# Optimization experiments

Hardware: AMD Instinct MI355X
Metric: run time of the kernel (lower is better)

The kernel has to match this reference:

```python
import jax, jax.numpy as jnp
import numpy as np
import math

D_MODEL = 512
KEY_DIM = 128
NUM_LAYERS = 2
TEMP = 30.0
NORM_EPS = 1e-5
NORM_SCALE = math.sqrt(1.0 / (D_MODEL * 4 * 4))


def _l2norm_lastdim(x):
    # F.normalize(x, p=2, dim=-1): x / max(||x||, 1e-12)
    n = jnp.sqrt(jnp.sum(x * x, axis=-1, keepdims=True))
    return x / jnp.maximum(n, 1e-12)


def _attn(q, k, v, WK, bK):
    # q: [Sq,B,D], k: [Sk,B,D], v: [Sk,B,D] -> [Sq,B,D]
    wq = _l2norm_lastdim(q @ WK + bK)            # [Sq,B,K]
    wk = _l2norm_lastdim(k @ WK + bK)            # [Sk,B,K]
    dot = jnp.einsum('qbk,sbk->bqs', wq, wk)     # cosine sims
    aff = jax.nn.softmax(dot * TEMP, axis=-1)
    return jnp.einsum('bqs,sbd->qbd', aff, v)


def _instance_norm(x, h, w):
    # x: [HW,B,D]; InstanceL2Norm over (D,h,w) per batch element, size_average=True
    HW, B, D = x.shape
    ss = jnp.sum(x * x, axis=(0, 2))             # [B]
    factor = NORM_SCALE * jnp.sqrt((D * h * w) / (ss + NORM_EPS))
    return x * factor[None, :, None]


def _encoder(src4d, WKs, bKs):
    B, D, H, W = src4d.shape
    x = src4d.reshape(B, D, H * W).transpose(2, 0, 1)   # [HW,B,D]
    for _ in range(NUM_LAYERS):
        x = _instance_norm(x + _attn(x, x, x, WKs, bKs), H, W)
    return x  # memory [HW,B,D]


def _decoder(tgt4d, memory, pos, WKs, bKs, WKc, bKc):
    B, D, H, W = tgt4d.shape
    x = tgt4d.reshape(B, D, H * W).transpose(2, 0, 1)   # [HW,B,D]
    for _ in range(NUM_LAYERS):
        x = _instance_norm(x + _attn(x, x, x, WKs, bKs), H, W)
        mask = _attn(x, memory, pos, WKc, bKc)
        t2 = _instance_norm(x * mask, H, W)
        t3 = _attn(x, memory, memory * pos, WKc, bKc)
        t4 = _instance_norm(x + t3, H, W)
        x = _instance_norm(t2 + t4, H, W)
    feat = x.reshape(H, W, B, D).transpose(2, 3, 0, 1)  # [B,D,H,W]
    return feat


def setup_inputs() -> dict:
    key = jax.random.key(0)
    k1, k2, k3, k4, k5 = jax.random.split(key, 5)
    B, D, H, W = 16, D_MODEL, 32, 32
    std = math.sqrt(2.0 / KEY_DIM)
    return {
        'train_feat': jax.random.normal(k1, (B, D, H, W), jnp.float32),
        'test_feat': jax.random.normal(k2, (B, D, H, W), jnp.float32),
        'train_label': jax.random.uniform(k3, (B, H, W), jnp.float32),
        'WK_self': jax.random.normal(k4, (D, KEY_DIM), jnp.float32) * std,
        'bK_self': jnp.zeros((KEY_DIM,), jnp.float32),
        'WK_cross': jax.random.normal(k5, (D, KEY_DIM), jnp.float32) * std,
        'bK_cross': jnp.zeros((KEY_DIM,), jnp.float32),
    }


def reference(train_feat, test_feat, train_label, WK_self, bK_self, WK_cross, bK_cross):
    B, D, H, W = train_feat.shape
    memory = _encoder(train_feat, WK_self, bK_self)              # [HW,B,D]
    # pos: label [B,H,W] -> [HW,B,1] -> broadcast to [HW,B,D]
    pos = jnp.broadcast_to(train_label.reshape(B, H * W).T[:, :, None], (H * W, B, D))
    encoded_feat = _decoder(train_feat, memory, pos, WK_self, bK_self, WK_cross, bK_cross)
    decoded_feat = _decoder(test_feat, memory, pos, WK_self, bK_self, WK_cross, bK_cross)
    return (encoded_feat, decoded_feat)
```

## Files before the change

### kernel.cpp

```cpp
#include <hip/hip_runtime.h>
#include <math.h>

#define NB 16
#define SEQ 1024
#define DM 512
#define KD 128
#define TEMP_F 30.0f
#define NS_F 0.011048543456039805f
#define DS_F 524288.0f

#define SS_IDX(grp, b) (((grp) * 32 + (b)) * 16)
#define SS_STRIDE 1536
#define SS_STAGES 12
#define SS_FLOATS (SS_STRIDE * SS_STAGES)

#define PSTR 72

typedef short bf16x8 __attribute__((ext_vector_type(8)));
typedef float f32x4 __attribute__((ext_vector_type(4)));
typedef unsigned short us;
typedef unsigned short us4v __attribute__((ext_vector_type(4)));
typedef unsigned short us8 __attribute__((ext_vector_type(8)));

__device__ __forceinline__ us f2bf(float x) {
    union { float f; unsigned u; } v; v.f = x;
    unsigned r = v.u + 0x7fffu + ((v.u >> 16) & 1u);
    return (us)(r >> 16);
}
__device__ __forceinline__ float bf2f(us h) {
    union { unsigned u; float f; } v; v.u = ((unsigned)h) << 16;
    return v.f;
}

#define GLL16(gp, lp) __builtin_amdgcn_global_load_lds( \
    (__attribute__((address_space(1))) void*)(unsigned long long)(gp), \
    (__attribute__((address_space(3))) void*)(unsigned)(unsigned long long)(lp), 16, 0, 0)

__global__ __launch_bounds__(256) void k_transpose_in(const float* __restrict__ src,
                                                      us* __restrict__ XC,
                                                      us* __restrict__ XT) {
    __shared__ float tile[32][33];
    const int b = blockIdx.z;
    const int d0 = blockIdx.x * 32;
    const int s0 = blockIdx.y * 32;
    const int tx = threadIdx.x, ty = threadIdx.y;
    const float* p = src + (size_t)b * DM * SEQ;
    us* pt = XT + (size_t)b * DM * SEQ;
    us* pc = XC + (size_t)b * SEQ * 1024;
#pragma unroll
    for (int j = 0; j < 32; j += 8) {
        const size_t o = (size_t)(d0 + ty + j) * SEQ + s0 + tx;
        const float v = p[o];
        tile[ty + j][tx] = v;
        pt[o] = f2bf(v);
    }
    __syncthreads();
#pragma unroll
    for (int j = 0; j < 4; ++j) {
        const int s = s0 + ty + j * 8;
        const int d = d0 + tx;
        const float v = tile[tx][ty + j * 8];
        const us h = f2bf(v);
        pc[(size_t)s * 1024 + d] = h;
        pc[(size_t)s * 1024 + 512 + d] = f2bf(v - bf2f(h));
    }
}

__global__ __launch_bounds__(256) void k_mklabel(const us* __restrict__ MT,
                                                 const float* __restrict__ label,
                                                 us* __restrict__ ML) {
    const int b = blockIdx.y;
    const size_t off = ((size_t)blockIdx.x * 256 + threadIdx.x) * 8;
    const int s = (int)(off & (SEQ - 1));
    const size_t o = (size_t)b * DM * SEQ + off;
    us8 v = *(const us8*)(MT + o);
    const float4 l0 = *(const float4*)(label + (size_t)b * SEQ + s);
    const float4 l1 = *(const float4*)(label + (size_t)b * SEQ + s + 4);
    us8 r;
    r[0] = f2bf(bf2f(v[0]) * l0.x); r[1] = f2bf(bf2f(v[1]) * l0.y);
    r[2] = f2bf(bf2f(v[2]) * l0.z); r[3] = f2bf(bf2f(v[3]) * l0.w);
    r[4] = f2bf(bf2f(v[4]) * l1.x); r[5] = f2bf(bf2f(v[5]) * l1.y);
    r[6] = f2bf(bf2f(v[6]) * l1.z); r[7] = f2bf(bf2f(v[7]) * l1.w);
    *(us8*)(ML + o) = r;
}

__global__ __launch_bounds__(256) void k_wsplit(const float* __restrict__ WK,
                                                us* __restrict__ WC) {
    const int k = blockIdx.x;
    for (int d = threadIdx.x; d < DM; d += 256) {
        const float v = WK[(size_t)d * KD + k];
        const us h = f2bf(v);
        WC[(size_t)k * 1024 + d] = h;
        WC[(size_t)k * 1024 + 512 + d] = f2bf(v - bf2f(h));
    }
}

__global__ __launch_bounds__(256) void k_proj(const us* __restrict__ XC,
                                              const us* __restrict__ WC,
                                              const float* __restrict__ bK,
                                              us* __restrict__ Wout) {
    const int row0 = blockIdx.x * 32;
    __shared__ short As[32 * 64], Bs[128 * 64];
    __shared__ float ssp[2][32];
    const int tid = threadIdx.x, w = tid >> 6, l = tid & 63;
    const int wm = (w >> 1) * 16, wn = (w & 1) * 64;
    const int sr = l >> 3, sc = (((l & 7) ^ (l >> 3)) << 3);
    const int lr = l & 15, lk = (l >> 4) * 8;
    const int sx = (lr & 7) << 3;
    f32x4 acc[4] = {};
    for (int k0 = 0; k0 < 1536; k0 += 64) {
        const int ak0 = (k0 < 1024) ? k0 : k0 - 1024;
        const int bk0 = (k0 < 512) ? k0 : k0 - 512;
        GLL16(XC + (size_t)(row0 + w * 8 + sr) * 1024 + ak0 + sc, &As[w * 512]);
#pragma unroll
        for (int cc = 0; cc < 4; ++cc) {
            const int c = 4 * w + cc;
            GLL16(WC + (size_t)(c * 8 + sr) * 1024 + bk0 + sc, &Bs[c * 512]);
        }
        __syncthreads();
#pragma unroll
        for (int kc = 0; kc < 2; ++kc) {
            const int kk = kc * 32 + lk;
            const bf16x8 a = *(const bf16x8*)&As[(wm + lr) * 64 + (kk ^ sx)];
            bf16x8 bb[4];
#pragma unroll
            for (int fn = 0; fn < 4; ++fn)
                bb[fn] = *(const bf16x8*)&Bs[(wn + fn * 16 + lr) * 64 + (kk ^ sx)];
#pragma unroll
            for (int fn = 0; fn < 4; ++fn)
                acc[fn] = __builtin_amdgcn_mfma_f32_16x16x32_bf16(a, bb[fn], acc[fn], 0, 0, 0);
        }
        __syncthreads();
    }
    const int er = l & 15, eq = (l >> 4) * 4;
    const int nh = w & 1;
    float bkv[4];
#pragma unroll
    for (int fn = 0; fn < 4; ++fn) bkv[fn] = bK[wn + fn * 16 + er];
    float vv[4][4];
#pragma unroll
    for (int r = 0; r < 4; ++r) {
        float ss = 0.f;
#pragma unroll
        for (int fn = 0; fn < 4; ++fn) {
            const float t = acc[fn][r] + bkv[fn];
            vv[fn][r] = t;
            ss += t * t;
        }
#pragma unroll
        for (int o = 8; o > 0; o >>= 1) ss += __shfl_xor(ss, o, 64);
        if (er == 0) ssp[nh][wm + eq + r] = ss;
    }
    __syncthreads();
#pragma unroll
    for (int r = 0; r < 4; ++r) {
        const int rowloc = wm + eq + r;
        const float tot = ssp[0][rowloc] + ssp[1][rowloc];
        const float invn = 1.0f / fmaxf(sqrtf(tot), 1e-12f);
        const size_t ro = (size_t)(row0 + rowloc) * 256;
#pragma unroll
        for (int fn = 0; fn < 4; ++fn) {
            const float ov = vv[fn][r] * invn;
            const us h = f2bf(ov);
            Wout[ro + wn + fn * 16 + er] = h;
            Wout[ro + 128 + wn + fn * 16 + er] = f2bf(ov - bf2f(h));
        }
    }
}

__global__ __launch_bounds__(512, 1) void k_attn(const us* __restrict__ Qc,
                                                 const us* __restrict__ Kc,
                                                 const us* __restrict__ VT,
                                                 const us* __restrict__ XC,
                                                 const float* __restrict__ labelp,
                                                 float* __restrict__ MVEC,
                                                 float* __restrict__ Cout,
                                                 float* __restrict__ SS, int mode, int kvmask) {
    const int b = blockIdx.x;
    const int bkv = b & kvmask;
    const int q0 = blockIdx.y * 64;
    __shared__ short KL[3][4 * 64 * 64];
    __shared__ us PL[2][64 * PSTR];
    __shared__ float RSL[2][64], RLL[2][64];
    __shared__ float INVL[64], MVL[64];
    __shared__ float ps[3][8];
    const int tid = threadIdx.x, w = tid >> 6, l = tid & 63;
    const int lr = l & 15, g = l >> 4, lk = g * 8;
    const int qa = w & 3, sh = w >> 2;
    const int kx = (lr & 7) << 3;
    const us* Qb = Qc + (size_t)b * SEQ * 256;
    const us* Kb = Kc + (size_t)bkv * SEQ * 256;
    const us* Vb = VT + (size_t)bkv * DM * SEQ;
    const float* Lb = labelp ? labelp + (size_t)(bkv & 15) * SEQ : nullptr;

    const us* Qrow = Qb + (size_t)(q0 + qa * 16 + lr) * 256;
    bf16x8 qh[4], ql[4];
#pragma unroll
    for (int kc = 0; kc < 4; ++kc) {
        qh[kc] = *(const bf16x8*)(Qrow + kc * 32 + lk);
        ql[kc] = *(const bf16x8*)(Qrow + 128 + kc * 32 + lk);
    }
#pragma unroll
    for (int t = 0; t < 2; ++t)
#pragma unroll
        for (int i = 0; i < 4; ++i) {
            const int c = w * 4 + i, p = c & 3, rg = c >> 2;
            GLL16(Kb + (size_t)(t * 64 + rg * 8 + (l >> 3)) * 256 + p * 64 + (((l & 7) ^ (l >> 3)) << 3),
                  &KL[t][p * 4096 + rg * 512 + l * 8]);
        }
    __syncthreads();

    f32x4 acc[4][4];
#pragma unroll
    for (int m = 0; m < 4; ++m)
#pragma unroll
        for (int n = 0; n < 4; ++n) acc[m][n] = (f32x4){0.f, 0.f, 0.f, 0.f};
    float rs = 0.f, rl = 0.f;
    int cur = 0;
    for (int it = 0; it < 16; ++it) {
        const int s0 = it * 64;
        const int pb = it & 1;
        bf16x8 vb0[4];
#pragma unroll
        for (int n = 0; n < 4; ++n)
            vb0[n] = *(const bf16x8*)(Vb + (size_t)(w * 64 + n * 16 + lr) * 1024 + s0 + lk);
        if (it < 14) {
            const int stg = (cur + 2 >= 3) ? cur - 1 : cur + 2;
            const int s2 = s0 + 128;
#pragma unroll
            for (int i = 0; i < 4; ++i) {
                const int c = w * 4 + i, p = c & 3, rg = c >> 2;
                GLL16(Kb + (size_t)(s2 + rg * 8 + (l >> 3)) * 256 + p * 64 + (((l & 7) ^ (l >> 3)) << 3),
                      &KL[stg][p * 4096 + rg * 512 + l * 8]);
            }
        }
        const short* KLc = KL[cur];
        bf16x8 kf[2][4];
#pragma unroll
        for (int sn = 0; sn < 2; ++sn)
#pragma unroll
            for (int kc = 0; kc < 4; ++kc)
                kf[sn][kc] = *(const bf16x8*)&KLc[(kc >> 1) * 4096 + (sh * 32 + sn * 16 + lr) * 64 +
                                                 ((((kc & 1) << 5) + lk) ^ kx)];
        f32x4 sA[2] = {}, sB[2] = {}, sC[2] = {};
        __builtin_amdgcn_s_setprio(1);
#pragma unroll
        for (int kc = 0; kc < 4; ++kc) {
            sA[0] = __builtin_amdgcn_mfma_f32_16x16x32_bf16(kf[0][kc], qh[kc], sA[0], 0, 0, 0);
            sA[1] = __builtin_amdgcn_mfma_f32_16x16x32_bf16(kf[1][kc], qh[kc], sA[1], 0, 0, 0);
            sB[0] = __builtin_amdgcn_mfma_f32_16x16x32_bf16(kf[0][kc], ql[kc], sB[0], 0, 0, 0);
            sB[1] = __builtin_amdgcn_mfma_f32_16x16x32_bf16(kf[1][kc], ql[kc], sB[1], 0, 0, 0);
        }
        __builtin_amdgcn_s_setprio(0);
#pragma unroll
        for (int sn = 0; sn < 2; ++sn)
#pragma unroll
            for (int kc = 0; kc < 4; ++kc)
                kf[sn][kc] = *(const bf16x8*)&KLc[(2 + (kc >> 1)) * 4096 + (sh * 32 + sn * 16 + lr) * 64 +
                                                 ((((kc & 1) << 5) + lk) ^ kx)];
        __builtin_amdgcn_s_setprio(1);
#pragma unroll
        for (int kc = 0; kc < 4; ++kc) {
            sC[0] = __builtin_amdgcn_mfma_f32_16x16x32_bf16(kf[0][kc], qh[kc], sC[0], 0, 0, 0);
            sC[1] = __builtin_amdgcn_mfma_f32_16x16x32_bf16(kf[1][kc], qh[kc], sC[1], 0, 0, 0);
        }
        __builtin_amdgcn_s_setprio(0);
#pragma unroll
        for (int sn = 0; sn < 2; ++sn) {
            const f32x4 sacc = sA[sn] + sB[sn] + sC[sn];
            const int sbase = sh * 32 + sn * 16 + g * 4;
            float lb4[4] = {0.f, 0.f, 0.f, 0.f};
            if (mode == 2) {
                const float4 t = *(const float4*)(Lb + s0 + sbase);
                lb4[0] = t.x; lb4[1] = t.y; lb4[2] = t.z; lb4[3] = t.w;
            }
            us4v pw;
#pragma unroll
            for (int r = 0; r < 4; ++r) {
                const float e = __expf(fmaf(TEMP_F, sacc[r], -TEMP_F));
                rs += e;
                rl += e * lb4[r];
                pw[r] = f2bf(e);
            }
            *(us4v*)&PL[pb][(qa * 16 + lr) * PSTR + sbase] = pw;
        }
        __syncthreads();
        bf16x8 vb1[4];
#pragma unroll
        for (int n = 0; n < 4; ++n)
            vb1[n] = *(const bf16x8*)(Vb + (size_t)(w * 64 + n * 16 + lr) * 1024 + s0 + 32 + lk);
        const us* PLc = PL[pb];
        bf16x8 pa[4];
#pragma unroll
        for (int m = 0; m < 4; ++m)
            pa[m] = *(const bf16x8*)&PLc[(m * 16 + lr) * PSTR + lk];
        __builtin_amdgcn_s_setprio(1);
#pragma unroll
        for (int m = 0; m < 4; ++m)
#pragma unroll
            for (int n = 0; n < 4; ++n)
                acc[m][n] = __builtin_amdgcn_mfma_f32_16x16x32_bf16(pa[m], vb0[n], acc[m][n], 0, 0, 0);
        __builtin_amdgcn_s_setprio(0);
#pragma unroll
        for (int m = 0; m < 4; ++m)
            pa[m] = *(const bf16x8*)&PLc[(m * 16 + lr) * PSTR + 32 + lk];
        __builtin_amdgcn_s_setprio(1);
#pragma unroll
        for (int m = 0; m < 4; ++m)
#pragma unroll
            for (int n = 0; n < 4; ++n)
                acc[m][n] = __builtin_amdgcn_mfma_f32_16x16x32_bf16(pa[m], vb1[n], acc[m][n], 0, 0, 0);
        __builtin_amdgcn_s_setprio(0);
        cur = (cur + 1 >= 3) ? 0 : cur + 1;
    }

    rs += __shfl_xor(rs, 16, 64);
    rs += __shfl_xor(rs, 32, 64);
    rl += __shfl_xor(rl, 16, 64);
    rl += __shfl_xor(rl, 32, 64);
    __syncthreads();
    if (g == 0) {
        RSL[sh][qa * 16 + lr] = rs;
        RLL[sh][qa * 16 + lr] = rl;
    }
    __syncthreads();
    if (tid < 64) {
        const float tot = RSL[0][tid] + RSL[1][tid];
        const float iv = 1.0f / tot;
        INVL[tid] = iv;
        const float mvv = (RLL[0][tid] + RLL[1][tid]) * iv;
        MVL[tid] = mvv;
        if (mode == 2) MVEC[(size_t)b * SEQ + q0 + tid] = mvv;
    }
    __syncthreads();

    const us* XCb = XC + (size_t)b * SEQ * 1024;
    float sa = 0.f, sb = 0.f, sab = 0.f;
#pragma unroll
    for (int m = 0; m < 4; ++m)
#pragma unroll
        for (int r = 0; r < 4; ++r) {
            const int q = m * 16 + g * 4 + r;
            const float iv = INVL[q];
            const float mvq = MVL[q];
            const int row = q0 + q;
#pragma unroll
            for (int n = 0; n < 4; ++n) {
                const int col = w * 64 + n * 16 + lr;
                float v = acc[m][n][r] * iv;
                const size_t o = ((size_t)b * SEQ + row) * DM + col;
                const size_t xo = (size_t)row * 1024 + col;
                const float x = bf2f(XCb[xo]) + bf2f(XCb[xo + 512]);
                v += x;
                sb += v * v;
                if (mode == 2) { const float a = x * mvq; sa += a * a; sab += a * v; }
                Cout[o] = v;
            }
        }
#pragma unroll
    for (int off = 32; off > 0; off >>= 1) {
        sb += __shfl_xor(sb, off, 64);
        if (mode == 2) { sa += __shfl_xor(sa, off, 64); sab += __shfl_xor(sab, off, 64); }
    }
    if (l == 0) { ps[0][w] = sb; ps[1][w] = sa; ps[2][w] = sab; }
    __syncthreads();
    if (tid == 0) {
        float t0 = 0.f, t1 = 0.f, t2 = 0.f;
#pragma unroll
        for (int i = 0; i < 8; ++i) { t0 += ps[0][i]; t1 += ps[1][i]; t2 += ps[2][i]; }
        if (mode == 1) {
            atomicAdd(&SS[SS_IDX(0, b)], t0);
        } else {
            atomicAdd(&SS[SS_IDX(0, b)], t1);
            atomicAdd(&SS[SS_IDX(1, b)], t0);
            atomicAdd(&SS[SS_IDX(2, b)], t2);
        }
    }
}

__global__ void k_zero(float* __restrict__ SSb) {
    const int i = blockIdx.x * 256 + threadIdx.x;
    if (i < SS_FLOATS) SSb[i] = 0.0f;
}

__global__ __launch_bounds__(256) void k_finish(const float* __restrict__ Tin,
                                                const us* __restrict__ XCin,
                                                const float* __restrict__ mv,
                                                const float* __restrict__ SS,
                                                us* __restrict__ XCout,
                                                us* __restrict__ XTb,
                                                float* __restrict__ XTf,
                                                int mode, int writeXC) {
    const int b = blockIdx.z;
    const int s0 = blockIdx.x * 32, d0 = blockIdx.y * 32;
    const int tx = threadIdx.x, ty = threadIdx.y;
    __shared__ float tile[32][33];
    float f1 = 0.f, f2 = 0.f, f3;
    if (mode == 0) {
        f3 = NS_F * sqrtf(DS_F / (SS[SS_IDX(0, b)] + 1e-5f));
    } else {
        const float ssa = SS[SS_IDX(0, b)], ssb = SS[SS_IDX(1, b)], ssab = SS[SS_IDX(2, b)];
        f1 = NS_F * sqrtf(DS_F / (ssa + 1e-5f));
        f2 = NS_F * sqrtf(DS_F / (ssb + 1e-5f));
        const float ssc = f1 * f1 * ssa + 2.f * f1 * f2 * ssab + f2 * f2 * ssb;
        f3 = NS_F * sqrtf(DS_F / (ssc + 1e-5f));
    }
#pragma unroll
    for (int j = 0; j < 4; ++j) {
        const int s = s0 + ty + j * 8;
        const int d = d0 + tx;
        const size_t o = ((size_t)b * SEQ + s) * DM + d;
        const size_t xo = ((size_t)b * SEQ + s) * 1024 + d;
        float v;
        if (mode == 0) v = f3 * Tin[o];
        else {
            const float x = bf2f(XCin[xo]) + bf2f(XCin[xo + 512]);
            v = f3 * (f1 * x * mv[(size_t)b * SEQ + s] + f2 * Tin[o]);
        }
        if (writeXC) {
            const us h = f2bf(v);
            XCout[xo] = h;
            XCout[xo + 512] = f2bf(v - bf2f(h));
        }
        tile[ty + j * 8][tx] = v;
    }
    __syncthreads();
#pragma unroll
    for (int j = 0; j < 4; ++j) {
        const int d = d0 + ty + j * 8;
        const int s = s0 + tx;
        const float v = tile[tx][ty + j * 8];
        const size_t o = ((size_t)b * DM + d) * SEQ + s;
        if (XTb) XTb[o] = f2bf(v);
        else if (XTf) XTf[o] = v;
    }
}

extern "C" void kernel_launch(void* const* d_in, const int* in_sizes, int n_in,
                              void* d_out, int out_size, void* d_ws, size_t ws_size,
                              hipStream_t stream) {
    const float* train_feat = (const float*)d_in[0];
    const float* test_feat  = (const float*)d_in[1];
    const float* label      = (const float*)d_in[2];
    const float* WKs        = (const float*)d_in[3];
    const float* bKs        = (const float*)d_in[4];
    const float* WKc        = (const float*)d_in[5];
    const float* bKc        = (const float*)d_in[6];
    float* out = (float*)d_out;
    float* w = (float*)d_ws;

    const size_t PB  = (size_t)SEQ * DM;
    const size_t SBD = (size_t)NB * PB;

    auto needF = [&](size_t nbat) {
        return nbat * (PB  + PB  + PB / 2  + PB / 4  + 1024 )
             + (size_t)NB * (PB / 2  + PB / 2  + PB / 4 )
             + 2 * (size_t)KD * 512  + SS_FLOATS + 4096;
    };
    const size_t wsf = ws_size / 4;
    const int nbat = (wsf >= needF(32)) ? 32 : NB;

    float* T    = w;
    us* XC      = (us*)(T + (size_t)nbat * PB);
    us* XTd     = XC + (size_t)nbat * 2 * PB;
    us* W1C     = XTd + (size_t)nbat * PB;
    us* MEMT    = W1C + (size_t)nbat * PB / 2;
    us* MEMLT   = MEMT + (size_t)NB * PB;
    us* WKMC    = MEMLT + (size_t)NB * PB;
    us* WCs     = WKMC + (size_t)NB * PB / 2;
    us* WCc     = WCs + (size_t)KD * 1024;
    float* MVEC = (float*)(WCc + (size_t)KD * 1024);
    float* SS   = MVEC + (size_t)nbat * SEQ;

    const dim3 gT_in(DM / 32, SEQ / 32, NB), bT(32, 8);

    int stage = 0;
    auto nextSS = [&]() { return SS + (size_t)(stage++) * SS_STRIDE; };

    k_zero<<<(SS_FLOATS + 255) / 256, 256, 0, stream>>>(SS);
    k_wsplit<<<KD, 256, 0, stream>>>(WKs, WCs);
    k_wsplit<<<KD, 256, 0, stream>>>(WKc, WCc);

    k_transpose_in<<<gT_in, bT, 0, stream>>>(train_feat, XC, MEMT);
    for (int l = 0; l < 2; ++l) {
        float* SSst = nextSS();
        k_proj<<<NB * SEQ / 32, 256, 0, stream>>>(XC, WCs, bKs, W1C);
        k_attn<<<dim3(NB, SEQ / 64), 512, 0, stream>>>(W1C, W1C, MEMT, XC, nullptr, nullptr, T, SSst, 1, 63);
        k_finish<<<dim3(SEQ / 32, DM / 32, NB), bT, 0, stream>>>(T, XC, nullptr, SSst, XC, MEMT, nullptr, 0, 1);
    }
    k_proj<<<NB * SEQ / 32, 256, 0, stream>>>(XC, WCc, bKc, WKMC);
    k_mklabel<<<dim3(DM * SEQ / 8 / 256, NB), 256, 0, stream>>>(MEMT, label, MEMLT);

    auto dec_layers = [&](int db, float* outp) {
        const dim3 gA(db, SEQ / 64);
        const dim3 gF(SEQ / 32, DM / 32, db);
        for (int l = 0; l < 2; ++l) {
            float* SSst = nextSS();
            k_proj<<<db * SEQ / 32, 256, 0, stream>>>(XC, WCs, bKs, W1C);
            k_attn<<<gA, 512, 0, stream>>>(W1C, W1C, XTd, XC, nullptr, nullptr, T, SSst, 1, 63);
            k_finish<<<gF, bT, 0, stream>>>(T, XC, nullptr, SSst, XC, XTd, nullptr, 0, 1);
            float* SSst2 = nextSS();
            k_proj<<<db * SEQ / 32, 256, 0, stream>>>(XC, WCc, bKc, W1C);
            k_attn<<<gA, 512, 0, stream>>>(W1C, WKMC, MEMLT, XC, label, MVEC, T, SSst2, 2, 15);
            if (l == 0)
                k_finish<<<gF, bT, 0, stream>>>(T, XC, MVEC, SSst2, XC, XTd, nullptr, 1, 1);
            else
                k_finish<<<gF, bT, 0, stream>>>(T, XC, MVEC, SSst2, XC, nullptr, outp, 1, 0);
        }
    };

    if (nbat == 32) {
        k_transpose_in<<<gT_in, bT, 0, stream>>>(train_feat, XC, XTd);
        k_transpose_in<<<gT_in, bT, 0, stream>>>(test_feat, XC + (size_t)NB * 2 * PB, XTd + (size_t)NB * PB);
        dec_layers(32, out);
    } else {
        k_transpose_in<<<gT_in, bT, 0, stream>>>(train_feat, XC, XTd);
        dec_layers(NB, out);
        k_transpose_in<<<gT_in, bT, 0, stream>>>(test_feat, XC, XTd);
        dec_layers(NB, out + SBD);
    }
}
```

Before: 871.0 us.

## Shrink attention LDS footprint to fit two blocks per CU

Replaces the three-stage K shared-memory ring with a two-stage double buffer and packs all shared arrays into one 80KB region. The P tile's row padding is replaced by an XOR swizzle, and the reduction scratch reuses the K buffer space. Launch bounds are raised to two blocks per CU so more blocks can be resident. In exchange, K is prefetched only one tile ahead instead of two, and the tighter register budget per thread risks spills.

```diff
diff --git a/kernel.cpp b/kernel.cpp
--- a/kernel.cpp
+++ b/kernel.cpp
@@ -13,8 +13,6 @@
 #define SS_STRIDE 1536
 #define SS_STAGES 12
 #define SS_FLOATS (SS_STRIDE * SS_STAGES)
-
-#define PSTR 72
 
 typedef short bf16x8 __attribute__((ext_vector_type(8)));
 typedef float f32x4 __attribute__((ext_vector_type(4)));
@@ -168,7 +166,7 @@
     }
 }
 
-__global__ __launch_bounds__(512, 1) void k_attn(const us* __restrict__ Qc,
+__global__ __launch_bounds__(512, 2) void k_attn(const us* __restrict__ Qc,
                                                  const us* __restrict__ Kc,
                                                  const us* __restrict__ VT,
                                                  const us* __restrict__ XC,
@@ -176,14 +174,11 @@
                                                  float* __restrict__ MVEC,
                                                  float* __restrict__ Cout,
                                                  float* __restrict__ SS, int mode, int kvmask) {
+    __shared__ __align__(16) char SMEM[81920];
+
     const int b = blockIdx.x;
     const int bkv = b & kvmask;
     const int q0 = blockIdx.y * 64;
-    __shared__ short KL[3][4 * 64 * 64];
-    __shared__ us PL[2][64 * PSTR];
-    __shared__ float RSL[2][64], RLL[2][64];
-    __shared__ float INVL[64], MVL[64];
-    __shared__ float ps[3][8];
     const int tid = threadIdx.x, w = tid >> 6, l = tid & 63;
     const int lr = l & 15, g = l >> 4, lk = g * 8;
     const int qa = w & 3, sh = w >> 2;
@@ -200,14 +195,15 @@
         qh[kc] = *(const bf16x8*)(Qrow + kc * 32 + lk);
         ql[kc] = *(const bf16x8*)(Qrow + 128 + kc * 32 + lk);
     }
-#pragma unroll
-    for (int t = 0; t < 2; ++t)
+    {
+        short* KL0 = (short*)SMEM;
 #pragma unroll
         for (int i = 0; i < 4; ++i) {
             const int c = w * 4 + i, p = c & 3, rg = c >> 2;
-            GLL16(Kb + (size_t)(t * 64 + rg * 8 + (l >> 3)) * 256 + p * 64 + (((l & 7) ^ (l >> 3)) << 3),
-                  &KL[t][p * 4096 + rg * 512 + l * 8]);
-        }
+            GLL16(Kb + (size_t)(rg * 8 + (l >> 3)) * 256 + p * 64 + (((l & 7) ^ (l >> 3)) << 3),
+                  &KL0[p * 4096 + rg * 512 + l * 8]);
+        }
+    }
     __syncthreads();
 
     f32x4 acc[4][4];
@@ -216,7 +212,6 @@
 #pragma unroll
         for (int n = 0; n < 4; ++n) acc[m][n] = (f32x4){0.f, 0.f, 0.f, 0.f};
     float rs = 0.f, rl = 0.f;
-    int cur = 0;
     for (int it = 0; it < 16; ++it) {
         const int s0 = it * 64;
         const int pb = it & 1;
@@ -224,17 +219,17 @@
 #pragma unroll
         for (int n = 0; n < 4; ++n)
             vb0[n] = *(const bf16x8*)(Vb + (size_t)(w * 64 + n * 16 + lr) * 1024 + s0 + lk);
-        if (it < 14) {
-            const int stg = (cur + 2 >= 3) ? cur - 1 : cur + 2;
-            const int s2 = s0 + 128;
+        if (it < 15) {
+            const int s1 = s0 + 64;
+            short* KLn = (short*)(SMEM + ((it + 1) & 1) * 32768);
 #pragma unroll
             for (int i = 0; i < 4; ++i) {
                 const int c = w * 4 + i, p = c & 3, rg = c >> 2;
-                GLL16(Kb + (size_t)(s2 + rg * 8 + (l >> 3)) * 256 + p * 64 + (((l & 7) ^ (l >> 3)) << 3),
-                      &KL[stg][p * 4096 + rg * 512 + l * 8]);
+                GLL16(Kb + (size_t)(s1 + rg * 8 + (l >> 3)) * 256 + p * 64 + (((l & 7) ^ (l >> 3)) << 3),
+                      &KLn[p * 4096 + rg * 512 + l * 8]);
             }
         }
-        const short* KLc = KL[cur];
+        const short* KLc = (const short*)(SMEM + (it & 1) * 32768);
         bf16x8 kf[2][4];
 #pragma unroll
         for (int sn = 0; sn < 2; ++sn)
@@ -265,6 +260,7 @@
             sC[1] = __builtin_amdgcn_mfma_f32_16x16x32_bf16(kf[1][kc], qh[kc], sC[1], 0, 0, 0);
         }
         __builtin_amdgcn_s_setprio(0);
+        us* PLw = (us*)(SMEM + 65536 + pb * 8192);
 #pragma unroll
         for (int sn = 0; sn < 2; ++sn) {
             const f32x4 sacc = sA[sn] + sB[sn] + sC[sn];
@@ -282,18 +278,18 @@
                 rl += e * lb4[r];
                 pw[r] = f2bf(e);
             }
-            *(us4v*)&PL[pb][(qa * 16 + lr) * PSTR + sbase] = pw;
+            *(us4v*)&PLw[(qa * 16 + lr) * 64 + (sbase ^ ((lr & 7) << 3))] = pw;
         }
         __syncthreads();
         bf16x8 vb1[4];
 #pragma unroll
         for (int n = 0; n < 4; ++n)
             vb1[n] = *(const bf16x8*)(Vb + (size_t)(w * 64 + n * 16 + lr) * 1024 + s0 + 32 + lk);
-        const us* PLc = PL[pb];
+        const us* PLc = (const us*)(SMEM + 65536 + pb * 8192);
         bf16x8 pa[4];
 #pragma unroll
         for (int m = 0; m < 4; ++m)
-            pa[m] = *(const bf16x8*)&PLc[(m * 16 + lr) * PSTR + lk];
+            pa[m] = *(const bf16x8*)&PLc[(m * 16 + lr) * 64 + (lk ^ ((lr & 7) << 3))];
         __builtin_amdgcn_s_setprio(1);
 #pragma unroll
         for (int m = 0; m < 4; ++m)
@@ -303,7 +299,7 @@
         __builtin_amdgcn_s_setprio(0);
 #pragma unroll
         for (int m = 0; m < 4; ++m)
-            pa[m] = *(const bf16x8*)&PLc[(m * 16 + lr) * PSTR + 32 + lk];
+            pa[m] = *(const bf16x8*)&PLc[(m * 16 + lr) * 64 + ((32 + lk) ^ ((lr & 7) << 3))];
         __builtin_amdgcn_s_setprio(1);
 #pragma unroll
         for (int m = 0; m < 4; ++m)
@@ -311,24 +307,28 @@
             for (int n = 0; n < 4; ++n)
                 acc[m][n] = __builtin_amdgcn_mfma_f32_16x16x32_bf16(pa[m], vb1[n], acc[m][n], 0, 0, 0);
         __builtin_amdgcn_s_setprio(0);
-        cur = (cur + 1 >= 3) ? 0 : cur + 1;
-    }
-
+    }
+
+    float* RED = (float*)SMEM;
+    float* RSL0 = RED;        float* RSL1 = RED + 64;
+    float* RLL0 = RED + 128;  float* RLL1 = RED + 192;
+    float* INVL = RED + 256;  float* MVL = RED + 320;
+    float* ps = RED + 384;
     rs += __shfl_xor(rs, 16, 64);
     rs += __shfl_xor(rs, 32, 64);
     rl += __shfl_xor(rl, 16, 64);
     rl += __shfl_xor(rl, 32, 64);
     __syncthreads();
     if (g == 0) {
-        RSL[sh][qa * 16 + lr] = rs;
-        RLL[sh][qa * 16 + lr] = rl;
+        (sh == 0 ? RSL0 : RSL1)[qa * 16 + lr] = rs;
+        (sh == 0 ? RLL0 : RLL1)[qa * 16 + lr] = rl;
     }
     __syncthreads();
     if (tid < 64) {
-        const float tot = RSL[0][tid] + RSL[1][tid];
+        const float tot = RSL0[tid] + RSL1[tid];
         const float iv = 1.0f / tot;
         INVL[tid] = iv;
-        const float mvv = (RLL[0][tid] + RLL[1][tid]) * iv;
+        const float mvv = (RLL0[tid] + RLL1[tid]) * iv;
         MVL[tid] = mvv;
         if (mode == 2) MVEC[(size_t)b * SEQ + q0 + tid] = mvv;
     }
@@ -362,12 +362,12 @@
         sb += __shfl_xor(sb, off, 64);
         if (mode == 2) { sa += __shfl_xor(sa, off, 64); sab += __shfl_xor(sab, off, 64); }
     }
-    if (l == 0) { ps[0][w] = sb; ps[1][w] = sa; ps[2][w] = sab; }
+    if (l == 0) { ps[0 * 8 + w] = sb; ps[1 * 8 + w] = sa; ps[2 * 8 + w] = sab; }
     __syncthreads();
     if (tid == 0) {
         float t0 = 0.f, t1 = 0.f, t2 = 0.f;
 #pragma unroll
-        for (int i = 0; i < 8; ++i) { t0 += ps[0][i]; t1 += ps[1][i]; t2 += ps[2][i]; }
+        for (int i = 0; i < 8; ++i) { t0 += ps[0 * 8 + i]; t1 += ps[1 * 8 + i]; t2 += ps[2 * 8 + i]; }
         if (mode == 1) {
             atomicAdd(&SS[SS_IDX(0, b)], t0);
         } else {
```

After: 872.7 us. No clear change (+0.2%).
